# Performance work log

Measured on AMD Instinct MI355X. Metric: run time of the kernel, lower is better.

Reference implementation:

```python
import jax, jax.numpy as jnp
import numpy as np
from jax import lax

B, C, HH, WW, M, DS = 16, 80, 128, 128, 32, 4
H_IMG, W_IMG = HH * DS, WW * DS


def setup_inputs() -> dict:
    key = jax.random.key(0)
    k = jax.random.split(key, 8)
    # head outputs: hm is sigmoid-activated in (0,1); sz/os are ReLU outputs (>=0)
    hm = jax.nn.sigmoid(jax.random.normal(k[0], (B, C, HH, WW), jnp.float32))
    sz = jax.random.uniform(k[1], (B, 2, HH, WW), jnp.float32) * 64.0
    os_ = jax.random.uniform(k[2], (B, 2, HH, WW), jnp.float32)
    # ground-truth boxes (xmin,ymin,xmax,ymax) inside the 512x512 image
    x1 = jax.random.uniform(k[3], (B, M), jnp.float32) * 440.0
    y1 = jax.random.uniform(k[4], (B, M), jnp.float32) * 440.0
    w = jax.random.uniform(k[5], (B, M), jnp.float32) * 60.0 + 8.0
    h = jax.random.uniform(k[6], (B, M), jnp.float32) * 60.0 + 8.0
    gt_bboxes = jnp.stack([x1, y1, x1 + w, y1 + h], -1)
    gt_classes = jax.random.randint(k[7], (B, M), 0, C, jnp.int32)
    return {"hm": hm, "sz": sz, "os": os_, "gt_bboxes": gt_bboxes, "gt_classes": gt_classes}


def _smooth_l1(p, g):
    d = jnp.abs(p - g)
    return jnp.where(d < 1.0, 0.5 * d * d, d - 0.5)


def reference(hm, sz, os, gt_bboxes, gt_classes):
    dt = hm.dtype
    # ---- NMS via 3x3 max-pool, keep only local maxima ----
    hmax = lax.reduce_window(hm, -jnp.inf, lax.max, (1, 1, 3, 3), (1, 1, 1, 1), "SAME")
    peaks = jnp.where(hm == hmax, hm, jnp.zeros((), dt)).transpose(0, 2, 3, 1)  # [B,H,W,C]
    values = peaks.max(-1)      # [B,H,W] best score per pixel
    idxs = peaks.argmax(-1)     # [B,H,W] class index
    keep = values > 0
    # ---- dense bbox decode (same math as the nonzero/gather loop, mask instead) ----
    szp = sz.transpose(0, 2, 3, 1)  # [B,H,W,2]
    osp = os.transpose(0, 2, 3, 1)
    pts = jnp.stack(jnp.meshgrid(jnp.arange(HH), jnp.arange(WW), indexing="ij"), -1).astype(dt)
    ctr = pts * DS + osp
    bb = jnp.concatenate([ctr - szp / 2, ctr + szp / 2], -1)  # [B,H,W,4]
    bboxes = jnp.stack([
        jnp.clip(bb[..., 0], 0.0, W_IMG), jnp.clip(bb[..., 1], 0.0, H_IMG),
        jnp.clip(bb[..., 2], 0.0, W_IMG), jnp.clip(bb[..., 3], 0.0, H_IMG)], -1)
    # ---- build gt heatmap / size / offset targets (vectorized gaussian splat) ----
    cxy = (gt_bboxes[..., :2] + gt_bboxes[..., 2:]) / 2          # [B,M,2]
    cpts = jnp.floor(cxy / DS)                                    # [B,M,2]
    sizes = gt_bboxes[..., 2:] - gt_bboxes[..., :2]               # [B,M,2]
    offs = cxy / DS - cpts                                        # [B,M,2]
    ci = cpts.astype(jnp.int32)
    bidx = jnp.broadcast_to(jnp.arange(B)[:, None], (B, M))
    gt_sz = jnp.zeros((B, HH, WW, 2), dt).at[bidx, ci[..., 0], ci[..., 1]].set(sizes)
    gt_os = jnp.zeros((B, HH, WW, 2), dt).at[bidx, ci[..., 0], ci[..., 1]].set(offs)
    sigma = sizes.max(-1) / DS                                    # [B,M] (note: not squared, as in source)
    d2 = ((pts[None, None] - cpts[:, :, None, None, :]) ** 2).sum(-1)   # [B,M,H,W]
    gauss = jnp.exp(-d2 / (2.0 * sigma[:, :, None, None]))
    seg = (bidx * C + gt_classes).reshape(-1)
    gt_hm = jax.ops.segment_max(gauss.reshape(B * M, HH, WW), seg, num_segments=B * C)
    gt_hm = jnp.maximum(gt_hm.reshape(B, C, HH, WW), 0.0)
    # ---- losses ----
    keep_tr = (gt_hm == 1.0).sum(1) > 0            # [B,H,W] center pixels
    n = keep_tr.sum().astype(dt)
    mask = keep_tr[..., None].astype(dt)
    size_loss = (_smooth_l1(szp, gt_sz) * mask).sum() / (2.0 * n) / n
    offset_loss = (_smooth_l1(osp, gt_os) * mask).sum() / (2.0 * n) / n
    fl = (1 - gt_hm) ** 4 * hm ** 2 * jnp.log1p(-hm) + gt_hm ** 4 * (1 - hm) ** 2 * jnp.log(hm)
    point_focal_loss = -fl.sum()
    return (values, idxs, bboxes, keep, point_focal_loss, size_loss, offset_loss, gt_hm)
```

## Files before the change

### kernel.cpp

```cpp
#include <hip/hip_runtime.h>
#include <math.h>

#define NB 16
#define NC 80
#define HH 128
#define WW 128
#define HW (HH*WW)
#define HW4 (HW/4)
#define NPIX (NB*HH*WW)
#define NM 32
#define IMG 512.0f

#define OFF_VALUES 0
#define OFF_IDXS   262144
#define OFF_BBOX   524288
#define OFF_KEEP   1572864
#define OFF_PFL    1835008
#define OFF_SZL    1835009
#define OFF_OSL    1835010
#define OFF_GTHM   1835011

struct BoxParam { float ci0, ci1, inv2sig; int cls; };

__device__ __forceinline__ float smooth_l1(float p, float g) {
    float d = fabsf(p - g);
    return (d < 1.0f) ? 0.5f * d * d : d - 0.5f;
}
__device__ __forceinline__ float fmax3(float a, float b, float c) {
    return fmaxf(fmaxf(a, b), c);
}

__global__ void setup_kernel(const float* __restrict__ gtb, const int* __restrict__ gtc,
                             BoxParam* __restrict__ bp, int* __restrict__ csr_start,
                             int* __restrict__ csr_order, float* __restrict__ out) {
    int t = threadIdx.x;
    if (t < NB * NM) {
        const float* g = gtb + t * 4;
        float x1 = g[0], y1 = g[1], x2 = g[2], y2 = g[3];
        float cx = (x1 + x2) * 0.5f, cy = (y1 + y2) * 0.5f;
        float c0 = floorf(cx * 0.25f);
        float c1 = floorf(cy * 0.25f);
        float w = x2 - x1, h = y2 - y1;
        float sigma = fmaxf(w, h) * 0.25f;
        BoxParam p;
        p.ci0 = c0; p.ci1 = c1;
        p.inv2sig = 1.0f / (2.0f * sigma);
        p.cls = gtc[t];
        bp[t] = p;
    }
    if (t == 0) out[OFF_PFL] = 0.0f;
    __syncthreads();
    if (t < NB) {
        int b = t;
        int base = b * NM;
        int cnt[NC + 1];
        for (int c = 0; c <= NC; ++c) cnt[c] = 0;
        for (int m = 0; m < NM; ++m) cnt[bp[base + m].cls + 1]++;
        for (int c = 0; c < NC; ++c) cnt[c + 1] += cnt[c];
        int* st = csr_start + b * (NC + 1);
        for (int c = 0; c <= NC; ++c) st[c] = cnt[c];
        int pos[NC];
        for (int c = 0; c < NC; ++c) pos[c] = cnt[c];
        for (int m = 0; m < NM; ++m) {
            int c = bp[base + m].cls;
            csr_order[base + pos[c]++] = m;
        }
    }
}

__launch_bounds__(256)
__global__ void main_kernel(const float* __restrict__ hm,
                            const BoxParam* __restrict__ bp,
                            const int* __restrict__ csr_start,
                            const int* __restrict__ csr_order,
                            float* __restrict__ pbest, int* __restrict__ pidx,
                            float* __restrict__ out, int lgG) {
    int blk = blockIdx.x;
    int G = 1 << lgG;
    int g = blk & (G - 1);
    int t2 = blk >> lgG;
    int b = t2 >> 4;
    int i0 = (t2 & 15) << 3;
    int tid = threadIdx.x;
    int row = tid >> 5;
    int jb  = (tid & 31) << 2;
    int i = i0 + row;
    int ncl = NC >> lgG;
    int c0 = g * ncl;

    __shared__ int   s_start[NC + 1];
    __shared__ float s_box[NM][3];
    __shared__ int   s_ord[NM];
    for (int k = tid; k < NC + 1; k += 256) s_start[k] = csr_start[b * (NC + 1) + k];
    if (tid < NM) {
        BoxParam p = bp[b * NM + tid];
        s_box[tid][0] = p.ci0; s_box[tid][1] = p.ci1; s_box[tid][2] = p.inv2sig;
        s_ord[tid] = csr_order[b * NM + tid];
    }
    __syncthreads();

    const float fi = (float)i, fjb = (float)jb;
    int iu  = (i > 0) ? i - 1 : 0;
    int idn = (i < HH - 1) ? i + 1 : HH - 1;
    size_t base = ((size_t)b * NC + c0) * HW;

    const float4* pC = (const float4*)(hm + base + i   * WW + jb);
    const float4* pU = (const float4*)(hm + base + iu  * WW + jb);
    const float4* pD = (const float4*)(hm + base + idn * WW + jb);
    float* gp = out + OFF_GTHM + base + i * WW + jb;

    int lane31 = tid & 31;
    bool clampL = (lane31 == 0);
    bool clampR = (lane31 == 31);

    float bestv[4] = {-1.f, -1.f, -1.f, -1.f};
    int   bestc[4] = {0, 0, 0, 0};
    float facc = 0.0f;

    auto process = [&](float4 cC, float4 cU, float4 cD, int c, float* gpc) {
        float h[4] = {cC.x, cC.y, cC.z, cC.w};
        float vm[4];
        vm[0] = fmax3(cU.x, h[0], cD.x);
        vm[1] = fmax3(cU.y, h[1], cD.y);
        vm[2] = fmax3(cU.z, h[2], cD.z);
        vm[3] = fmax3(cU.w, h[3], cD.w);
        float left  = __shfl_up(vm[3], 1);
        float right = __shfl_down(vm[0], 1);
        if (clampL) left  = vm[0];
        if (clampR) right = vm[3];
        float mx[4];
        mx[0] = fmax3(left,  vm[0], vm[1]);
        mx[1] = fmax3(vm[0], vm[1], vm[2]);
        mx[2] = fmax3(vm[1], vm[2], vm[3]);
        mx[3] = fmax3(vm[2], vm[3], right);
        #pragma unroll
        for (int k = 0; k < 4; ++k) {
            float p = (h[k] >= mx[k]) ? h[k] : 0.0f;
            if (p > bestv[k]) { bestv[k] = p; bestc[k] = c; }
        }

        int s0 = s_start[c], s1 = s_start[c + 1];
        if (s0 == s1) {
            __builtin_nontemporal_store(0.0f, gpc + 0);
            __builtin_nontemporal_store(0.0f, gpc + 1);
            __builtin_nontemporal_store(0.0f, gpc + 2);
            __builtin_nontemporal_store(0.0f, gpc + 3);
            #pragma unroll
            for (int k = 0; k < 4; ++k)
                facc += h[k] * h[k] * __logf(1.0f - h[k]);
        } else {
            float gv[4] = {0.f, 0.f, 0.f, 0.f};
            for (int kk = s0; kk < s1; ++kk) {
                int m = s_ord[kk];
                float d0 = fi - s_box[m][0];
                float nis = -s_box[m][2];
                float dj = fjb - s_box[m][1];
                float e = d0 * d0;
                #pragma unroll
                for (int k = 0; k < 4; ++k) {
                    float d1 = dj + (float)k;
                    gv[k] = fmaxf(gv[k], __expf((e + d1 * d1) * nis));
                }
            }
            __builtin_nontemporal_store(gv[0], gpc + 0);
            __builtin_nontemporal_store(gv[1], gpc + 1);
            __builtin_nontemporal_store(gv[2], gpc + 2);
            __builtin_nontemporal_store(gv[3], gpc + 3);
            #pragma unroll
            for (int k = 0; k < 4; ++k) {
                float hk = h[k], ohk = 1.0f - hk;
                float gk = gv[k], omk = 1.0f - gk;
                float om2 = omk * omk, g2 = gk * gk;
                facc += (om2 * om2) * hk * hk * __logf(ohk)
                      + (g2 * g2) * ohk * ohk * __logf(hk);
            }
        }
    };

    float4 cC = *pC, cU = *pU, cD = *pD;
    for (int cc = 0; cc < ncl - 1; ++cc) {
        float4 nC = pC[HW4], nU = pU[HW4], nD = pD[HW4];
        process(cC, cU, cD, c0 + cc, gp);
        pC += HW4; pU += HW4; pD += HW4; gp += HW;
        cC = nC; cU = nU; cD = nD;
    }
    process(cC, cU, cD, c0 + ncl - 1, gp);

    int pixbase = (b * HH + i) * WW + jb;
    float4 bsv = {bestv[0], bestv[1], bestv[2], bestv[3]};
    int4   bci = {bestc[0], bestc[1], bestc[2], bestc[3]};
    *(float4*)(pbest + (size_t)g * NPIX + pixbase) = bsv;
    *(int4*)  (pidx  + (size_t)g * NPIX + pixbase) = bci;

    #pragma unroll
    for (int off = 32; off > 0; off >>= 1) facc += __shfl_down(facc, off);
    __shared__ float s_red[4];
    if ((tid & 63) == 0) s_red[tid >> 6] = facc;
    __syncthreads();
    if (tid == 0)
        atomicAdd(out + OFF_PFL, -(s_red[0] + s_red[1] + s_red[2] + s_red[3]));
}

__global__ void combine_kernel(const float* __restrict__ pbest, const int* __restrict__ pidx,
                               const float* __restrict__ sz, const float* __restrict__ osr,
                               float* __restrict__ out, int G) {
    int p4 = blockIdx.x * 256 + threadIdx.x;
    int px = p4 << 2;
    float bv[4] = {-1.f, -1.f, -1.f, -1.f};
    int   bi[4] = {0, 0, 0, 0};
    for (int g = 0; g < G; ++g) {
        float4 v = *(const float4*)(pbest + (size_t)g * NPIX + px);
        int4  ix = *(const int4*)  (pidx  + (size_t)g * NPIX + px);
        float vv[4] = {v.x, v.y, v.z, v.w};
        int   ii[4] = {ix.x, ix.y, ix.z, ix.w};
        #pragma unroll
        for (int k = 0; k < 4; ++k)
            if (vv[k] > bv[k]) { bv[k] = vv[k]; bi[k] = ii[k]; }
    }
    float4 vals = {bv[0], bv[1], bv[2], bv[3]};
    float4 idxf = {(float)bi[0], (float)bi[1], (float)bi[2], (float)bi[3]};
    float4 keep = {bv[0] > 0.f ? 1.f : 0.f, bv[1] > 0.f ? 1.f : 0.f,
                   bv[2] > 0.f ? 1.f : 0.f, bv[3] > 0.f ? 1.f : 0.f};
    *(float4*)(out + OFF_VALUES + px) = vals;
    *(float4*)(out + OFF_IDXS + px)   = idxf;
    *(float4*)(out + OFF_KEEP + px)   = keep;

    int b = px >> 14, ij = px & 16383;
    float fi = (float)(ij >> 7), fjb = (float)(ij & 127);
    const float* szb = sz  + (size_t)b * 2 * HW;
    const float* osb = osr + (size_t)b * 2 * HW;
    float4 s0v = *(const float4*)(szb + ij);
    float4 s1v = *(const float4*)(szb + HW + ij);
    float4 o0v = *(const float4*)(osb + ij);
    float4 o1v = *(const float4*)(osb + HW + ij);
    float s0a[4] = {s0v.x, s0v.y, s0v.z, s0v.w};
    float s1a[4] = {s1v.x, s1v.y, s1v.z, s1v.w};
    float o0a[4] = {o0v.x, o0v.y, o0v.z, o0v.w};
    float o1a[4] = {o1v.x, o1v.y, o1v.z, o1v.w};
    #pragma unroll
    for (int k = 0; k < 4; ++k) {
        float cx = fi * 4.0f + o0a[k];
        float cy = (fjb + (float)k) * 4.0f + o1a[k];
        float4 bb;
        bb.x = fminf(fmaxf(cx - s0a[k] * 0.5f, 0.0f), IMG);
        bb.y = fminf(fmaxf(cy - s1a[k] * 0.5f, 0.0f), IMG);
        bb.z = fminf(fmaxf(cx + s0a[k] * 0.5f, 0.0f), IMG);
        bb.w = fminf(fmaxf(cy + s1a[k] * 0.5f, 0.0f), IMG);
        reinterpret_cast<float4*>(out + OFF_BBOX)[px + k] = bb;
    }
}

__global__ void loss_kernel(const float* __restrict__ gtb, const float* __restrict__ sz,
                            const float* __restrict__ osr, float* __restrict__ out) {
    int t = threadIdx.x;
    int b = t >> 5, m = t & 31;
    __shared__ int s_ci[NB * NM];
    const float* g = gtb + t * 4;
    float x1 = g[0], y1 = g[1], x2 = g[2], y2 = g[3];
    float cx = (x1 + x2) * 0.5f, cy = (y1 + y2) * 0.5f;
    float c0f = floorf(cx * 0.25f), c1f = floorf(cy * 0.25f);
    int ci0 = (int)c0f, ci1 = (int)c1f;
    s_ci[t] = ci0 * WW + ci1;
    __syncthreads();

    bool winner = true;
    int mycell = s_ci[t];
    for (int m2 = m + 1; m2 < NM; ++m2)
        if (s_ci[b * NM + m2] == mycell) { winner = false; break; }

    float nloc = 0.0f, szs = 0.0f, oss = 0.0f;
    if (winner) {
        nloc = 1.0f;
        float w = x2 - x1, h = y2 - y1;
        float offx = cx * 0.25f - c0f, offy = cy * 0.25f - c1f;
        size_t pb = (size_t)b * 2 * HW + (size_t)ci0 * WW + ci1;
        float ps0 = sz[pb], ps1 = sz[pb + HW];
        float po0 = osr[pb], po1 = osr[pb + HW];
        szs = smooth_l1(ps0, w) + smooth_l1(ps1, h);
        oss = smooth_l1(po0, offx) + smooth_l1(po1, offy);
    }

    #pragma unroll
    for (int off = 32; off > 0; off >>= 1) {
        nloc += __shfl_down(nloc, off);
        szs  += __shfl_down(szs, off);
        oss  += __shfl_down(oss, off);
    }
    __shared__ float red[8][3];
    int wid = t >> 6;
    if ((t & 63) == 0) { red[wid][0] = nloc; red[wid][1] = szs; red[wid][2] = oss; }
    __syncthreads();
    if (t == 0) {
        float n = 0.0f, ss = 0.0f, os_ = 0.0f;
        for (int w2 = 0; w2 < 8; ++w2) { n += red[w2][0]; ss += red[w2][1]; os_ += red[w2][2]; }
        out[OFF_SZL] = ss / (2.0f * n) / n;
        out[OFF_OSL] = os_ / (2.0f * n) / n;
    }
}

extern "C" void kernel_launch(void* const* d_in, const int* in_sizes, int n_in,
                              void* d_out, int out_size, void* d_ws, size_t ws_size,
                              hipStream_t stream) {
    const float* hm  = (const float*)d_in[0];
    const float* sz  = (const float*)d_in[1];
    const float* osr = (const float*)d_in[2];
    const float* gtb = (const float*)d_in[3];
    const int*   gtc = (const int*)d_in[4];
    float* out = (float*)d_out;

    BoxParam* bp   = (BoxParam*)d_ws;
    int* csr_start = (int*)((char*)d_ws + 8192);
    int* csr_order = (int*)((char*)d_ws + 13376);

    size_t need4 = 16384 + (size_t)4 * NPIX * 8;
    size_t need2 = 16384 + (size_t)2 * NPIX * 8;
    int lgG = (ws_size >= need4) ? 2 : (ws_size >= need2) ? 1 : 0;
    int G = 1 << lgG;
    float* ws_best;
    int*   ws_idx;
    if (lgG > 0) {
        ws_best = (float*)((char*)d_ws + 16384);
        ws_idx  = (int*)((char*)d_ws + 16384 + (size_t)G * NPIX * 4);
    } else {
        ws_best = out + OFF_VALUES;
        ws_idx  = (int*)(out + OFF_IDXS);
    }

    setup_kernel<<<1, 512, 0, stream>>>(gtb, gtc, bp, csr_start, csr_order, out);
    main_kernel<<<NB * 16 * G, 256, 0, stream>>>(hm, bp, csr_start, csr_order,
                                                 ws_best, ws_idx, out, lgG);
    combine_kernel<<<NPIX / 4 / 256, 256, 0, stream>>>(ws_best, ws_idx, sz, osr, out, G);
    loss_kernel<<<1, 512, 0, stream>>>(gtb, sz, osr, out);
}
```

Before: 68.32 us.

## Split classes 8 ways and merge per-pixel argmax via packed 64-bit atomicMax

Raises the class split of the main kernel from at most 4 to a fixed 8 groups, giving more blocks to fill the GPU. Per-group best value and class are packed into a 64-bit key and merged with atomicMax into one buffer, which a combined zero/setup kernel clears first. The combine kernel then reads one packed value per pixel instead of G partial buffers. The focal-loss float atomic is replaced by per-block partials summed in the loss kernel. Costs are an extra zeroing pass, 64-bit atomics per pixel, and a fixed workspace layout that no longer checks ws_size. Reversing the class index inside the key keeps the lowest class on ties, matching argmax.

```diff
diff --git a/kernel.cpp b/kernel.cpp
--- a/kernel.cpp
+++ b/kernel.cpp
@@ -10,6 +10,9 @@
 #define NPIX (NB*HH*WW)
 #define NM 32
 #define IMG 512.0f
+#define G8 8
+#define NCL (NC/G8)
+#define MAIN_BLOCKS (NB*16*G8)
 
 #define OFF_VALUES 0
 #define OFF_IDXS   262144
@@ -20,6 +23,12 @@
 #define OFF_OSL    1835010
 #define OFF_GTHM   1835011
 
+#define WS_BP    0
+#define WS_CSRS  8192
+#define WS_CSRO  13376
+#define WS_FPART 15424
+#define WS_PACK  24576
+
 struct BoxParam { float ci0, ci1, inv2sig; int cls; };
 
 __device__ __forceinline__ float smooth_l1(float p, float g) {
@@ -30,11 +39,15 @@
     return fmaxf(fmaxf(a, b), c);
 }
 
-__global__ void setup_kernel(const float* __restrict__ gtb, const int* __restrict__ gtc,
-                             BoxParam* __restrict__ bp, int* __restrict__ csr_start,
-                             int* __restrict__ csr_order, float* __restrict__ out) {
-    int t = threadIdx.x;
-    if (t < NB * NM) {
+__global__ void zero_setup_kernel(const float* __restrict__ gtb, const int* __restrict__ gtc,
+                                  BoxParam* __restrict__ bp, int* __restrict__ csr_start,
+                                  int* __restrict__ csr_order,
+                                  unsigned long long* __restrict__ packed) {
+    int gt = blockIdx.x * 256 + threadIdx.x;
+    packed[gt] = 0ULL;
+    if (blockIdx.x != 0) return;
+    int t0 = threadIdx.x;
+    for (int t = t0; t < NB * NM; t += 256) {
         const float* g = gtb + t * 4;
         float x1 = g[0], y1 = g[1], x2 = g[2], y2 = g[3];
         float cx = (x1 + x2) * 0.5f, cy = (y1 + y2) * 0.5f;
@@ -48,10 +61,9 @@
         p.cls = gtc[t];
         bp[t] = p;
     }
-    if (t == 0) out[OFF_PFL] = 0.0f;
-    __syncthreads();
-    if (t < NB) {
-        int b = t;
+    __syncthreads();
+    if (t0 < NB) {
+        int b = t0;
         int base = b * NM;
         int cnt[NC + 1];
         for (int c = 0; c <= NC; ++c) cnt[c] = 0;
@@ -68,25 +80,24 @@
     }
 }
 
-__launch_bounds__(256)
+__launch_bounds__(256, 8)
 __global__ void main_kernel(const float* __restrict__ hm,
                             const BoxParam* __restrict__ bp,
                             const int* __restrict__ csr_start,
                             const int* __restrict__ csr_order,
-                            float* __restrict__ pbest, int* __restrict__ pidx,
-                            float* __restrict__ out, int lgG) {
+                            unsigned long long* __restrict__ packed,
+                            float* __restrict__ fpart,
+                            float* __restrict__ out) {
     int blk = blockIdx.x;
-    int G = 1 << lgG;
-    int g = blk & (G - 1);
-    int t2 = blk >> lgG;
+    int g = blk & (G8 - 1);
+    int t2 = blk >> 3;
     int b = t2 >> 4;
     int i0 = (t2 & 15) << 3;
     int tid = threadIdx.x;
     int row = tid >> 5;
     int jb  = (tid & 31) << 2;
     int i = i0 + row;
-    int ncl = NC >> lgG;
-    int c0 = g * ncl;
+    int c0 = g * NCL;
 
     __shared__ int   s_start[NC + 1];
     __shared__ float s_box[NM][3];
@@ -178,19 +189,22 @@
     };
 
     float4 cC = *pC, cU = *pU, cD = *pD;
-    for (int cc = 0; cc < ncl - 1; ++cc) {
+    for (int cc = 0; cc < NCL - 1; ++cc) {
         float4 nC = pC[HW4], nU = pU[HW4], nD = pD[HW4];
         process(cC, cU, cD, c0 + cc, gp);
         pC += HW4; pU += HW4; pD += HW4; gp += HW;
         cC = nC; cU = nU; cD = nD;
     }
-    process(cC, cU, cD, c0 + ncl - 1, gp);
+    process(cC, cU, cD, c0 + NCL - 1, gp);
 
     int pixbase = (b * HH + i) * WW + jb;
-    float4 bsv = {bestv[0], bestv[1], bestv[2], bestv[3]};
-    int4   bci = {bestc[0], bestc[1], bestc[2], bestc[3]};
-    *(float4*)(pbest + (size_t)g * NPIX + pixbase) = bsv;
-    *(int4*)  (pidx  + (size_t)g * NPIX + pixbase) = bci;
+    #pragma unroll
+    for (int k = 0; k < 4; ++k) {
+        unsigned long long pk =
+            ((unsigned long long)__float_as_uint(bestv[k]) << 32) |
+            (unsigned int)(NC - 1 - bestc[k]);
+        atomicMax(packed + pixbase + k, pk);
+    }
 
     #pragma unroll
     for (int off = 32; off > 0; off >>= 1) facc += __shfl_down(facc, off);
@@ -198,24 +212,22 @@
     if ((tid & 63) == 0) s_red[tid >> 6] = facc;
     __syncthreads();
     if (tid == 0)
-        atomicAdd(out + OFF_PFL, -(s_red[0] + s_red[1] + s_red[2] + s_red[3]));
-}
-
-__global__ void combine_kernel(const float* __restrict__ pbest, const int* __restrict__ pidx,
+        fpart[blk] = s_red[0] + s_red[1] + s_red[2] + s_red[3];
+}
+
+__global__ void combine_kernel(const unsigned long long* __restrict__ packed,
                                const float* __restrict__ sz, const float* __restrict__ osr,
-                               float* __restrict__ out, int G) {
+                               float* __restrict__ out) {
     int p4 = blockIdx.x * 256 + threadIdx.x;
     int px = p4 << 2;
-    float bv[4] = {-1.f, -1.f, -1.f, -1.f};
-    int   bi[4] = {0, 0, 0, 0};
-    for (int g = 0; g < G; ++g) {
-        float4 v = *(const float4*)(pbest + (size_t)g * NPIX + px);
-        int4  ix = *(const int4*)  (pidx  + (size_t)g * NPIX + px);
-        float vv[4] = {v.x, v.y, v.z, v.w};
-        int   ii[4] = {ix.x, ix.y, ix.z, ix.w};
-        #pragma unroll
-        for (int k = 0; k < 4; ++k)
-            if (vv[k] > bv[k]) { bv[k] = vv[k]; bi[k] = ii[k]; }
+    ulonglong2 pa = *(const ulonglong2*)(packed + px);
+    ulonglong2 pb = *(const ulonglong2*)(packed + px + 2);
+    unsigned long long pk[4] = {pa.x, pa.y, pb.x, pb.y};
+    float bv[4]; int bi[4];
+    #pragma unroll
+    for (int k = 0; k < 4; ++k) {
+        bv[k] = __uint_as_float((unsigned int)(pk[k] >> 32));
+        bi[k] = NC - 1 - (int)(unsigned int)(pk[k] & 0xffffffffu);
     }
     float4 vals = {bv[0], bv[1], bv[2], bv[3]};
     float4 idxf = {(float)bi[0], (float)bi[1], (float)bi[2], (float)bi[3]};
@@ -251,7 +263,8 @@
 }
 
 __global__ void loss_kernel(const float* __restrict__ gtb, const float* __restrict__ sz,
-                            const float* __restrict__ osr, float* __restrict__ out) {
+                            const float* __restrict__ osr, const float* __restrict__ fpart,
+                            float* __restrict__ out) {
     int t = threadIdx.x;
     int b = t >> 5, m = t & 31;
     __shared__ int s_ci[NB * NM];
@@ -280,21 +293,25 @@
         oss = smooth_l1(po0, offx) + smooth_l1(po1, offy);
     }
 
+    float fsum = fpart[t] + fpart[t + 512] + fpart[t + 1024] + fpart[t + 1536];
+
     #pragma unroll
     for (int off = 32; off > 0; off >>= 1) {
         nloc += __shfl_down(nloc, off);
         szs  += __shfl_down(szs, off);
         oss  += __shfl_down(oss, off);
-    }
-    __shared__ float red[8][3];
+        fsum += __shfl_down(fsum, off);
+    }
+    __shared__ float red[8][4];
     int wid = t >> 6;
-    if ((t & 63) == 0) { red[wid][0] = nloc; red[wid][1] = szs; red[wid][2] = oss; }
+    if ((t & 63) == 0) { red[wid][0] = nloc; red[wid][1] = szs; red[wid][2] = oss; red[wid][3] = fsum; }
     __syncthreads();
     if (t == 0) {
-        float n = 0.0f, ss = 0.0f, os_ = 0.0f;
-        for (int w2 = 0; w2 < 8; ++w2) { n += red[w2][0]; ss += red[w2][1]; os_ += red[w2][2]; }
+        float n = 0.0f, ss = 0.0f, os_ = 0.0f, ft = 0.0f;
+        for (int w2 = 0; w2 < 8; ++w2) { n += red[w2][0]; ss += red[w2][1]; os_ += red[w2][2]; ft += red[w2][3]; }
         out[OFF_SZL] = ss / (2.0f * n) / n;
         out[OFF_OSL] = os_ / (2.0f * n) / n;
+        out[OFF_PFL] = -ft;
     }
 }
 
@@ -308,27 +325,14 @@
     const int*   gtc = (const int*)d_in[4];
     float* out = (float*)d_out;
 
-    BoxParam* bp   = (BoxParam*)d_ws;
-    int* csr_start = (int*)((char*)d_ws + 8192);
-    int* csr_order = (int*)((char*)d_ws + 13376);
-
-    size_t need4 = 16384 + (size_t)4 * NPIX * 8;
-    size_t need2 = 16384 + (size_t)2 * NPIX * 8;
-    int lgG = (ws_size >= need4) ? 2 : (ws_size >= need2) ? 1 : 0;
-    int G = 1 << lgG;
-    float* ws_best;
-    int*   ws_idx;
-    if (lgG > 0) {
-        ws_best = (float*)((char*)d_ws + 16384);
-        ws_idx  = (int*)((char*)d_ws + 16384 + (size_t)G * NPIX * 4);
-    } else {
-        ws_best = out + OFF_VALUES;
-        ws_idx  = (int*)(out + OFF_IDXS);
-    }
-
-    setup_kernel<<<1, 512, 0, stream>>>(gtb, gtc, bp, csr_start, csr_order, out);
-    main_kernel<<<NB * 16 * G, 256, 0, stream>>>(hm, bp, csr_start, csr_order,
-                                                 ws_best, ws_idx, out, lgG);
-    combine_kernel<<<NPIX / 4 / 256, 256, 0, stream>>>(ws_best, ws_idx, sz, osr, out, G);
-    loss_kernel<<<1, 512, 0, stream>>>(gtb, sz, osr, out);
-}
+    BoxParam* bp   = (BoxParam*)((char*)d_ws + WS_BP);
+    int* csr_start = (int*)((char*)d_ws + WS_CSRS);
+    int* csr_order = (int*)((char*)d_ws + WS_CSRO);
+    float* fpart   = (float*)((char*)d_ws + WS_FPART);
+    unsigned long long* packed = (unsigned long long*)((char*)d_ws + WS_PACK);
+
+    zero_setup_kernel<<<NPIX / 256, 256, 0, stream>>>(gtb, gtc, bp, csr_start, csr_order, packed);
+    main_kernel<<<MAIN_BLOCKS, 256, 0, stream>>>(hm, bp, csr_start, csr_order, packed, fpart, out);
+    combine_kernel<<<NPIX / 4 / 256, 256, 0, stream>>>(packed, sz, osr, out);
+    loss_kernel<<<1, 512, 0, stream>>>(gtb, sz, osr, fpart, out);
+}
```

New measurement: 94.27 us. 38.0% more time.
